# Kernel optimization log

Hardware: AMD Instinct MI355X
Metric: run time of the kernel (lower is better)

The kernel has to match this reference:

```python
import jax, jax.numpy as jnp
import numpy as np

B, T, D, K = 16, 4096, 512, 128
ALPHA_MIN = 1e-06
OMEGA_MAX = float(np.pi)
SN_EPS = 1e-06


def setup_inputs() -> dict:
    key = jax.random.key(0)
    ks = jax.random.split(key, 7)
    x = jax.random.normal(ks[0], (B, T, D), jnp.float32)
    # irregular positive step sizes, mean ~ 1/T like the uniform-grid default
    dt = jax.random.uniform(ks[1], (B, T), jnp.float32, minval=0.1, maxval=1.9) * (1.0 / T)
    # replicate reset_parameters: target_alpha ~ U(0.01, 0.2), raw = log(expm1(alpha - alpha_min))
    target_alpha = jax.random.uniform(ks[2], (K,), jnp.float32, minval=0.01, maxval=0.2)
    s_real_raw = jnp.log(jnp.expm1(jnp.maximum(target_alpha - ALPHA_MIN, 1e-08)))
    s_imag = jax.random.uniform(ks[3], (K,), jnp.float32, minval=-np.pi, maxval=np.pi)
    # kaiming-uniform-ish proj weight [K, D] and bias [K]
    W = jax.random.normal(ks[4], (K, D), jnp.float32) * (1.0 / np.sqrt(D))
    bound = 1.0 / np.sqrt(D)
    bias = jax.random.uniform(ks[5], (K,), jnp.float32, minval=-bound, maxval=bound)
    b_log = jnp.zeros((K,), jnp.float32)  # torch stores [1,1,K]; broadcasting is identical
    u_sn = jax.random.normal(ks[6], (K,), jnp.float32)  # spectral-norm power-iteration vector
    return {"x": x, "dt": dt, "s_real_raw": s_real_raw, "s_imag": s_imag,
            "W": W, "bias": bias, "b_log": b_log, "u_sn": u_sn}


def _spectral_normalize(W, u):
    # one power iteration, u/v detached (as torch.nn.utils.spectral_norm does)
    v = W.T @ u
    v = v / (jnp.linalg.norm(v) + SN_EPS)
    u2 = W @ v
    u2 = u2 / (jnp.linalg.norm(u2) + SN_EPS)
    u2 = jax.lax.stop_gradient(u2)
    v = jax.lax.stop_gradient(v)
    sigma = u2 @ (W @ v)
    return W / sigma


def reference(x, dt, s_real_raw, s_imag, W, bias, b_log, u_sn):
    # x: [B,T,D], dt: [B,T] -> lap_feats [B,T,2K]
    alpha = jax.nn.softplus(s_real_raw) + ALPHA_MIN          # [K] strictly positive decay
    omega = jnp.clip(s_imag, -OMEGA_MAX, OMEGA_MAX)          # [K]
    Wsn = _spectral_normalize(W, u_sn)
    u = jnp.einsum('btd,kd->btk', x, Wsn) + bias             # spectral-norm projection
    dt3 = dt[..., None]                                      # [B,T,1]
    rho = jnp.exp(-alpha * dt3)                              # [B,T,K]
    theta = omega * dt3
    cos_t, sin_t = jnp.cos(theta), jnp.sin(theta)
    b_gain = jnp.exp(b_log)                                  # [K]
    inj = (1.0 - rho) * (b_gain * u)                         # [B,T,K]

    def step(carry, inp):
        c, s = carry
        r, ct, st, it = inp
        c_new = r * (c * ct - s * st) + it
        s_new = r * (c * st + s * ct) + it
        return (c_new, s_new), (c_new, s_new)

    seq = (jnp.moveaxis(rho, 1, 0), jnp.moveaxis(cos_t, 1, 0),
           jnp.moveaxis(sin_t, 1, 0), jnp.moveaxis(inj, 1, 0))  # each [T,B,K]
    init = (jnp.zeros((x.shape[0], K), x.dtype), jnp.zeros((x.shape[0], K), x.dtype))
    _, (C, S) = jax.lax.scan(step, init, seq)
    C = jnp.moveaxis(C, 0, 1)  # [B,T,K]
    S = jnp.moveaxis(S, 0, 1)
    return jnp.concatenate([C, S], axis=-1)
```

## Files before the change

### kernel.cpp

```cpp
#include <hip/hip_runtime.h>
#include <stdint.h>

#define BB 16
#define TT 4096
#define DDIM 512
#define KK 128
#define TCB 128
#define NCB (TT / TCB)
#define PI_F 3.14159265358979323846f

typedef unsigned short u16;
typedef __attribute__((ext_vector_type(8))) short short8;
typedef __attribute__((ext_vector_type(4))) float f32x4;

__device__ __forceinline__ uint32_t cvt_bf16_rn(float f) {
  uint32_t u = __float_as_uint(f);
  return (u + 0x7FFFu + ((u >> 16) & 1u)) >> 16;
}
__device__ __forceinline__ uint32_t pack2(float a, float b) {
  return cvt_bf16_rn(a) | (cvt_bf16_rn(b) << 16);
}
__device__ __forceinline__ short8 pack8s(float4 f0, float4 f1) {
  uint4 u;
  u.x = pack2(f0.x, f0.y);
  u.y = pack2(f0.z, f0.w);
  u.z = pack2(f1.x, f1.y);
  u.w = pack2(f1.z, f1.w);
  return __builtin_bit_cast(short8, u);
}

__global__ __launch_bounds__(256) void k_prep(
    const float* __restrict__ W, const float* __restrict__ u_sn,
    const float* __restrict__ s_real_raw, const float* __restrict__ s_imag,
    const float* __restrict__ bias, const float* __restrict__ b_log,
    const float* __restrict__ dt,
    float* __restrict__ params, u16* __restrict__ Wp2, float* __restrict__ ct) {
  int gb = blockIdx.x;
  int tid = threadIdx.x;
  if (gb < 64) {
    int idx = gb * 256 + tid;
    int o = idx * 4;
    int lent = o >> 3;
    int half = (o >> 2) & 1;
    int ks = lent >> 9;
    int rem = lent & 511;
    int kg = rem >> 6;
    int l = rem & 63;
    int k = kg * 16 + (l & 15);
    int d = ks * 32 + (l >> 4) * 8 + half * 4;
    float4 v = *(const float4*)&W[(size_t)k * DDIM + d];
    uint2 p;
    p.x = pack2(v.x, v.y);
    p.y = pack2(v.z, v.w);
    *(uint2*)&Wp2[o] = p;
  } else if (gb < 80) {
    __shared__ float sc[256];
    int b = gb - 64;
    const float* row = dt + (size_t)b * TT;
    float* orow = ct + (size_t)b * TT;
    float loc[16];
    float s = 0.f;
    int base = tid * 16;
    for (int i = 0; i < 16; ++i) { s += row[base + i]; loc[i] = s; }
    sc[tid] = s;
    __syncthreads();
    for (int off = 1; off < 256; off <<= 1) {
      float v = (tid >= off) ? sc[tid - off] : 0.f;
      __syncthreads();
      sc[tid] += v;
      __syncthreads();
    }
    float excl = sc[tid] - s;
    for (int i = 0; i < 16; ++i) orow[base + i] = excl + loc[i];
  } else {
    __shared__ float su[KK];
    __shared__ float sv[DDIM];
    __shared__ float red[4];
    __shared__ float wred[256];
    __shared__ float s_sig;
    if (tid < KK) su[tid] = u_sn[tid];
    __syncthreads();
    for (int rep = 0; rep < 2; ++rep) {
      int d = tid + rep * 256;
      float acc = 0.f;
      for (int k = 0; k < KK; ++k) acc += W[k * DDIM + d] * su[k];
      sv[d] = acc;
    }
    __syncthreads();
    float nn = 0.f;
    for (int rep = 0; rep < 2; ++rep) { float v = sv[tid + rep * 256]; nn += v * v; }
    for (int off = 32; off > 0; off >>= 1) nn += __shfl_down(nn, off, 64);
    if ((tid & 63) == 0) red[tid >> 6] = nn;
    __syncthreads();
    float vn2 = red[0] + red[1] + red[2] + red[3];
    __syncthreads();
    float vinv = 1.f / (sqrtf(vn2) + 1e-6f);
    for (int rep = 0; rep < 2; ++rep) sv[tid + rep * 256] *= vinv;
    __syncthreads();
    {
      int k = tid & 127, q = tid >> 7;
      const float* wrow = W + (size_t)k * DDIM + q * 256;
      float p = 0.f;
      for (int d = 0; d < 256; ++d) p += wrow[d] * sv[q * 256 + d];
      wred[tid] = p;
    }
    __syncthreads();
    float wv = 0.f;
    if (tid < KK) wv = wred[tid] + wred[tid + 128];
    float q = wv * wv;
    for (int off = 32; off > 0; off >>= 1) q += __shfl_down(q, off, 64);
    if ((tid & 63) == 0) red[tid >> 6] = q;
    __syncthreads();
    if (tid == 0) {
      float wn2 = red[0] + red[1] + red[2] + red[3];
      s_sig = wn2 / (sqrtf(wn2) + 1e-6f);
    }
    __syncthreads();
    if (tid < KK) {
      float inv_sigma = 1.f / s_sig;
      float sr = s_real_raw[tid];
      float alpha = ((sr > 20.f) ? sr : log1pf(expf(sr))) + 1e-6f;
      float om = fminf(fmaxf(s_imag[tid], -PI_F), PI_F);
      float bg = expf(b_log[tid]);
      params[tid] = alpha;
      params[KK + tid] = om;
      params[2 * KK + tid] = bg * inv_sigma;
      params[3 * KK + tid] = bg * bias[tid];
    }
  }
}

__global__ __launch_bounds__(512, 4) void k_gemm(
    const float* __restrict__ x, const u16* __restrict__ Wp2,
    const float* __restrict__ dt, const float* __restrict__ ct,
    const float* __restrict__ params, u16* __restrict__ itvb,
    float* __restrict__ csum_re, float* __restrict__ csum_im) {
  __shared__ __align__(16) u16 smem[18432];

  const int chunk = blockIdx.x, b = blockIdx.y;
  const int tid = threadIdx.x;
  const int wv = tid >> 6, l = tid & 63;
  const int lm = l & 15, lg = l >> 4;
  const int kw = wv & 1, tw = wv >> 1;
  const int t0 = chunk * TCB;

  const float* xA0 = x + ((size_t)b * TT + t0 + tw * 32 + lm) * DDIM + lg * 8;
  const float* xA1 = xA0 + (size_t)16 * DDIM;
  const u16* wB = Wp2 + (size_t)(kw * 4) * 512 + l * 8;

  f32x4 acc[2][4];
#pragma unroll
  for (int m = 0; m < 2; ++m)
#pragma unroll
    for (int n = 0; n < 4; ++n) acc[m][n] = (f32x4)(0.0f);

#pragma unroll 4
  for (int ks = 0; ks < 16; ++ks) {
    float4 a00 = *(const float4*)(xA0 + ks * 32);
    float4 a01 = *(const float4*)(xA0 + ks * 32 + 4);
    float4 a10 = *(const float4*)(xA1 + ks * 32);
    float4 a11 = *(const float4*)(xA1 + ks * 32 + 4);
    short8 fb[4];
#pragma unroll
    for (int n = 0; n < 4; ++n)
      fb[n] = *(const short8*)(wB + (size_t)(ks * 8 + n) * 512);
    short8 fa[2];
    fa[0] = pack8s(a00, a01);
    fa[1] = pack8s(a10, a11);
#pragma unroll
    for (int m = 0; m < 2; ++m)
#pragma unroll
      for (int n = 0; n < 4; ++n)
        acc[m][n] = __builtin_amdgcn_mfma_f32_16x16x32_bf16(fa[m], fb[n], acc[m][n], 0, 0, 0);
  }

  u16* litv = smem;
  float* totr = (float*)(smem + 16384);
  float* toti = totr + 512;

  float dtv[2][4], ctv[2][4];
#pragma unroll
  for (int m = 0; m < 2; ++m)
#pragma unroll
    for (int r = 0; r < 4; ++r) {
      int t = t0 + tw * 32 + m * 16 + lg * 4 + r;
      dtv[m][r] = dt[(size_t)b * TT + t];
      ctv[m][r] = ct[(size_t)b * TT + t];
    }

#pragma unroll
  for (int n = 0; n < 4; ++n) {
    int k = kw * 64 + n * 16 + lm;
    float pal = params[k], pom = params[KK + k];
    float pc1 = params[2 * KK + k], pc2 = params[3 * KK + k];
    float sr = 0.f, si2 = 0.f;
#pragma unroll
    for (int m = 0; m < 2; ++m)
#pragma unroll
      for (int r = 0; r < 4; ++r) {
        float g = acc[m][n][r];
        float a = pal * dtv[m][r];
        float omr = a * (1.f - a * (0.5f - a * (1.f / 6.f)));
        float itv = omr * (pc1 * g + pc2);
        int tl = tw * 32 + m * 16 + lg * 4 + r;
        litv[tl * KK + k] = (u16)cvt_bf16_rn(itv);
        float e = __expf(pal * ctv[m][r]);
        float sn, cs;
        __sincosf(pom * ctv[m][r], &sn, &cs);
        sr += itv * e * cs;
        si2 -= itv * e * sn;
      }
    sr += __shfl_xor(sr, 16, 64);
    sr += __shfl_xor(sr, 32, 64);
    si2 += __shfl_xor(si2, 16, 64);
    si2 += __shfl_xor(si2, 32, 64);
    if (lg == 0) { totr[tw * KK + k] = sr; toti[tw * KK + k] = si2; }
  }
  __syncthreads();

  if (tid < 256) {
    int v = tid & 127;
    float* src = (tid < 128) ? totr : toti;
    float* dst = (tid < 128) ? csum_re : csum_im;
    dst[((size_t)b * NCB + chunk) * KK + v] =
        (src[v] + src[KK + v]) + (src[2 * KK + v] + src[3 * KK + v]);
  }
  {
    int row = tid >> 4;
    int c8 = (tid & 15) * 8;
#pragma unroll
    for (int rr = 0; rr < 4; ++rr) {
      int tr = rr * 32 + row;
      uint4 v = *(const uint4*)&litv[tr * KK + c8];
      *(uint4*)&itvb[((size_t)b * TT + t0 + tr) * KK + c8] = v;
    }
  }
}

__global__ __launch_bounds__(512) void k_final(
    const u16* __restrict__ itvb, const float* __restrict__ ct,
    const float* __restrict__ params,
    const float* __restrict__ csum_re, const float* __restrict__ csum_im,
    float* __restrict__ out) {
  __shared__ float prer[KK], prei[KK];
  __shared__ float segr[16][KK], segi[16][KK];
  const int chunk = blockIdx.x, b = blockIdx.y;
  const int tid = threadIdx.x;
  const int k4 = (tid & 31) * 4, tseg = tid >> 5;
  const int tbase = chunk * TCB + tseg * 8;

  if (tid < 256) {
    int v = tid & 127;
    const float* srcp = (tid < 128) ? csum_re : csum_im;
    float* dstp = (tid < 128) ? prer : prei;
    size_t base = (size_t)b * NCB * KK + v;
    float a0 = 0.f, a1 = 0.f, a2 = 0.f, a3 = 0.f;
    int c = 0;
    for (; c + 4 <= chunk; c += 4) {
      a0 += srcp[base + (size_t)(c + 0) * KK];
      a1 += srcp[base + (size_t)(c + 1) * KK];
      a2 += srcp[base + (size_t)(c + 2) * KK];
      a3 += srcp[base + (size_t)(c + 3) * KK];
    }
    for (; c < chunk; ++c) a0 += srcp[base + (size_t)c * KK];
    dstp[v] = (a0 + a1) + (a2 + a3);
  }

  float4 pal4 = *(const float4*)&params[k4];
  float4 pom4 = *(const float4*)&params[KK + k4];
  float pal[4] = {pal4.x, pal4.y, pal4.z, pal4.w};
  float pom[4] = {pom4.x, pom4.y, pom4.z, pom4.w};

  uint2 iv8[8];
  float fr[8][4], fi[8][4];
  float sr[4] = {0.f, 0.f, 0.f, 0.f}, si[4] = {0.f, 0.f, 0.f, 0.f};
#pragma unroll
  for (int i = 0; i < 8; ++i) {
    int t = tbase + i;
    float ctv = ct[(size_t)b * TT + t];
    iv8[i] = *(const uint2*)&itvb[((size_t)b * TT + t) * KK + k4];
    float it[4] = {__uint_as_float(iv8[i].x << 16), __uint_as_float(iv8[i].x & 0xFFFF0000u),
                   __uint_as_float(iv8[i].y << 16), __uint_as_float(iv8[i].y & 0xFFFF0000u)};
#pragma unroll
    for (int c = 0; c < 4; ++c) {
      float e = __expf(pal[c] * ctv);
      float sn, cs;
      __sincosf(pom[c] * ctv, &sn, &cs);
      fr[i][c] = e * cs;
      fi[i][c] = e * sn;
      sr[c] += it[c] * fr[i][c];
      si[c] -= it[c] * fi[i][c];
    }
  }
  *(float4*)&segr[tseg][k4] = make_float4(sr[0], sr[1], sr[2], sr[3]);
  *(float4*)&segi[tseg][k4] = make_float4(si[0], si[1], si[2], si[3]);
  __syncthreads();
  float cr[4], ci[4];
  {
    float4 p0 = *(const float4*)&prer[k4];
    float4 p1 = *(const float4*)&prei[k4];
    cr[0] = p0.x; cr[1] = p0.y; cr[2] = p0.z; cr[3] = p0.w;
    ci[0] = p1.x; ci[1] = p1.y; ci[2] = p1.z; ci[3] = p1.w;
  }
  for (int s = 0; s < tseg; ++s) {
    float4 a = *(const float4*)&segr[s][k4];
    float4 bb = *(const float4*)&segi[s][k4];
    cr[0] += a.x; cr[1] += a.y; cr[2] += a.z; cr[3] += a.w;
    ci[0] += bb.x; ci[1] += bb.y; ci[2] += bb.z; ci[3] += bb.w;
  }
#pragma unroll
  for (int i = 0; i < 8; ++i) {
    int t = tbase + i;
    float it[4] = {__uint_as_float(iv8[i].x << 16), __uint_as_float(iv8[i].x & 0xFFFF0000u),
                   __uint_as_float(iv8[i].y << 16), __uint_as_float(iv8[i].y & 0xFFFF0000u)};
    float C4[4], S4[4];
#pragma unroll
    for (int c = 0; c < 4; ++c) {
      float f_r = fr[i][c], f_i = fi[i][c];
      cr[c] += it[c] * f_r;
      ci[c] -= it[c] * f_i;
      float inv = __builtin_amdgcn_rcpf(f_r * f_r + f_i * f_i);
      float Rw = (cr[c] * f_r - ci[c] * f_i) * inv;
      float Iw = (cr[c] * f_i + ci[c] * f_r) * inv;
      C4[c] = Rw - Iw;
      S4[c] = Rw + Iw;
    }
    size_t rowb = ((size_t)b * TT + t) * (2 * KK);
    *(float4*)&out[rowb + k4] = make_float4(C4[0], C4[1], C4[2], C4[3]);
    *(float4*)&out[rowb + KK + k4] = make_float4(S4[0], S4[1], S4[2], S4[3]);
  }
}

extern "C" void kernel_launch(void* const* d_in, const int* in_sizes, int n_in,
                              void* d_out, int out_size, void* d_ws, size_t ws_size,
                              hipStream_t stream) {
  const float* x    = (const float*)d_in[0];
  const float* dt   = (const float*)d_in[1];
  const float* srr  = (const float*)d_in[2];
  const float* si   = (const float*)d_in[3];
  const float* W    = (const float*)d_in[4];
  const float* bias = (const float*)d_in[5];
  const float* blog = (const float*)d_in[6];
  const float* usn  = (const float*)d_in[7];
  float* out = (float*)d_out;
  float* ws = (float*)d_ws;

  float* params  = ws;
  float* ct      = ws + 4 * KK;
  float* csum_re = ct + (size_t)BB * TT;
  float* csum_im = csum_re + (size_t)BB * NCB * KK;
  u16*   Wp2     = (u16*)(csum_im + (size_t)BB * NCB * KK);
  u16*   itvb    = Wp2 + 65536;

  k_prep<<<81, 256, 0, stream>>>(W, usn, srr, si, bias, blog, dt, params, Wp2, ct);
  k_gemm<<<dim3(NCB, BB), 512, 0, stream>>>(x, Wp2, dt, ct, params, itvb,
                                            csum_re, csum_im);
  k_final<<<dim3(NCB, BB), 512, 0, stream>>>(itvb, ct, params,
                                             csum_re, csum_im, out);
}
```

Measured before the change: 82.67 us.

## Stage x tile in swizzled LDS and halve GEMM chunk size

The GEMM kernel now takes 64-timestep chunks instead of 128, which doubles its grid, and splits K across four waves instead of two. Each block first loads its x tile with coalesced reads, converts it to bf16 and writes it to LDS with an XOR swizzle. The MFMA loop then reads A fragments from LDS instead of doing strided global loads per lane. The final kernel keeps 128-step chunks and sums twice as many partial carry chunks. This costs more LDS per block (64KB) and two extra barriers, which may lower occupancy.

```diff
diff --git a/kernel.cpp b/kernel.cpp
--- a/kernel.cpp
+++ b/kernel.cpp
@@ -5,8 +5,10 @@
 #define TT 4096
 #define DDIM 512
 #define KK 128
-#define TCB 128
-#define NCB (TT / TCB)
+#define TCA 64
+#define NCA (TT / TCA)
+#define TCF 128
+#define NCF (TT / TCF)
 #define PI_F 3.14159265358979323846f
 
 typedef unsigned short u16;
@@ -20,13 +22,13 @@
 __device__ __forceinline__ uint32_t pack2(float a, float b) {
   return cvt_bf16_rn(a) | (cvt_bf16_rn(b) << 16);
 }
-__device__ __forceinline__ short8 pack8s(float4 f0, float4 f1) {
+__device__ __forceinline__ uint4 pack8u(float4 f0, float4 f1) {
   uint4 u;
   u.x = pack2(f0.x, f0.y);
   u.y = pack2(f0.z, f0.w);
   u.z = pack2(f1.x, f1.y);
   u.w = pack2(f1.z, f1.w);
-  return __builtin_bit_cast(short8, u);
+  return u;
 }
 
 __global__ __launch_bounds__(256) void k_prep(
@@ -135,48 +137,60 @@
     const float* __restrict__ dt, const float* __restrict__ ct,
     const float* __restrict__ params, u16* __restrict__ itvb,
     float* __restrict__ csum_re, float* __restrict__ csum_im) {
-  __shared__ __align__(16) u16 smem[18432];
-
-  const int chunk = blockIdx.x, b = blockIdx.y;
+  __shared__ __align__(16) u16 smem[32768];
+
+  const int ca = blockIdx.x, b = blockIdx.y;
   const int tid = threadIdx.x;
   const int wv = tid >> 6, l = tid & 63;
   const int lm = l & 15, lg = l >> 4;
-  const int kw = wv & 1, tw = wv >> 1;
-  const int t0 = chunk * TCB;
-
-  const float* xA0 = x + ((size_t)b * TT + t0 + tw * 32 + lm) * DDIM + lg * 8;
-  const float* xA1 = xA0 + (size_t)16 * DDIM;
-  const u16* wB = Wp2 + (size_t)(kw * 4) * 512 + l * 8;
-
-  f32x4 acc[2][4];
+  const int kw = wv & 3, tw = wv >> 2;
+  const int t0 = ca * TCA;
+
+  {
+    const float* xb0 = x + ((size_t)b * TT + t0) * DDIM;
+#pragma unroll
+    for (int i = 0; i < 8; ++i) {
+      int g = i * 512 + tid;
+      int t = g >> 6, c8 = g & 63;
+      int tile = c8 >> 3, dl8 = c8 & 7;
+      float4 v0 = *(const float4*)(xb0 + (size_t)t * DDIM + c8 * 8);
+      float4 v1 = *(const float4*)(xb0 + (size_t)t * DDIM + c8 * 8 + 4);
+      *(uint4*)&smem[tile * 4096 + t * 64 + ((dl8 ^ (t & 7)) << 3)] = pack8u(v0, v1);
+    }
+  }
+  __syncthreads();
+
+  f32x4 acc[2][2];
 #pragma unroll
   for (int m = 0; m < 2; ++m)
 #pragma unroll
-    for (int n = 0; n < 4; ++n) acc[m][n] = (f32x4)(0.0f);
-
+    for (int n = 0; n < 2; ++n) acc[m][n] = (f32x4)(0.0f);
+
+  const u16* wB = Wp2 + (size_t)(kw * 2) * 512 + l * 8;
 #pragma unroll 4
   for (int ks = 0; ks < 16; ++ks) {
-    float4 a00 = *(const float4*)(xA0 + ks * 32);
-    float4 a01 = *(const float4*)(xA0 + ks * 32 + 4);
-    float4 a10 = *(const float4*)(xA1 + ks * 32);
-    float4 a11 = *(const float4*)(xA1 + ks * 32 + 4);
-    short8 fb[4];
-#pragma unroll
-    for (int n = 0; n < 4; ++n)
+    short8 fb[2];
+#pragma unroll
+    for (int n = 0; n < 2; ++n)
       fb[n] = *(const short8*)(wB + (size_t)(ks * 8 + n) * 512);
     short8 fa[2];
-    fa[0] = pack8s(a00, a01);
-    fa[1] = pack8s(a10, a11);
+#pragma unroll
+    for (int m = 0; m < 2; ++m) {
+      int row = tw * 32 + m * 16 + lm;
+      int sw = (((ks & 1) * 4 + lg) ^ (row & 7)) * 8;
+      fa[m] = *(const short8*)&smem[(ks >> 1) * 4096 + row * 64 + sw];
+    }
 #pragma unroll
     for (int m = 0; m < 2; ++m)
 #pragma unroll
-      for (int n = 0; n < 4; ++n)
+      for (int n = 0; n < 2; ++n)
         acc[m][n] = __builtin_amdgcn_mfma_f32_16x16x32_bf16(fa[m], fb[n], acc[m][n], 0, 0, 0);
   }
+  __syncthreads();
 
   u16* litv = smem;
-  float* totr = (float*)(smem + 16384);
-  float* toti = totr + 512;
+  float* totr = (float*)(smem + 8192);
+  float* toti = totr + 256;
 
   float dtv[2][4], ctv[2][4];
 #pragma unroll
@@ -189,8 +203,8 @@
     }
 
 #pragma unroll
-  for (int n = 0; n < 4; ++n) {
-    int k = kw * 64 + n * 16 + lm;
+  for (int n = 0; n < 2; ++n) {
+    int k = kw * 32 + n * 16 + lm;
     float pal = params[k], pom = params[KK + k];
     float pc1 = params[2 * KK + k], pc2 = params[3 * KK + k];
     float sr = 0.f, si2 = 0.f;
@@ -222,14 +236,13 @@
     int v = tid & 127;
     float* src = (tid < 128) ? totr : toti;
     float* dst = (tid < 128) ? csum_re : csum_im;
-    dst[((size_t)b * NCB + chunk) * KK + v] =
-        (src[v] + src[KK + v]) + (src[2 * KK + v] + src[3 * KK + v]);
+    dst[((size_t)b * NCA + ca) * KK + v] = src[v] + src[KK + v];
   }
   {
     int row = tid >> 4;
     int c8 = (tid & 15) * 8;
 #pragma unroll
-    for (int rr = 0; rr < 4; ++rr) {
+    for (int rr = 0; rr < 2; ++rr) {
       int tr = rr * 32 + row;
       uint4 v = *(const uint4*)&litv[tr * KK + c8];
       *(uint4*)&itvb[((size_t)b * TT + t0 + tr) * KK + c8] = v;
@@ -247,22 +260,23 @@
   const int chunk = blockIdx.x, b = blockIdx.y;
   const int tid = threadIdx.x;
   const int k4 = (tid & 31) * 4, tseg = tid >> 5;
-  const int tbase = chunk * TCB + tseg * 8;
+  const int tbase = chunk * TCF + tseg * 8;
 
   if (tid < 256) {
     int v = tid & 127;
     const float* srcp = (tid < 128) ? csum_re : csum_im;
     float* dstp = (tid < 128) ? prer : prei;
-    size_t base = (size_t)b * NCB * KK + v;
+    size_t base = (size_t)b * NCA * KK + v;
+    int lim = 2 * chunk;
     float a0 = 0.f, a1 = 0.f, a2 = 0.f, a3 = 0.f;
     int c = 0;
-    for (; c + 4 <= chunk; c += 4) {
+    for (; c + 4 <= lim; c += 4) {
       a0 += srcp[base + (size_t)(c + 0) * KK];
       a1 += srcp[base + (size_t)(c + 1) * KK];
       a2 += srcp[base + (size_t)(c + 2) * KK];
       a3 += srcp[base + (size_t)(c + 3) * KK];
     }
-    for (; c < chunk; ++c) a0 += srcp[base + (size_t)c * KK];
+    for (; c < lim; ++c) a0 += srcp[base + (size_t)c * KK];
     dstp[v] = (a0 + a1) + (a2 + a3);
   }
 
@@ -348,13 +362,13 @@
   float* params  = ws;
   float* ct      = ws + 4 * KK;
   float* csum_re = ct + (size_t)BB * TT;
-  float* csum_im = csum_re + (size_t)BB * NCB * KK;
-  u16*   Wp2     = (u16*)(csum_im + (size_t)BB * NCB * KK);
+  float* csum_im = csum_re + (size_t)BB * NCA * KK;
+  u16*   Wp2     = (u16*)(csum_im + (size_t)BB * NCA * KK);
   u16*   itvb    = Wp2 + 65536;
 
   k_prep<<<81, 256, 0, stream>>>(W, usn, srr, si, bias, blog, dt, params, Wp2, ct);
-  k_gemm<<<dim3(NCB, BB), 512, 0, stream>>>(x, Wp2, dt, ct, params, itvb,
+  k_gemm<<<dim3(NCA, BB), 512, 0, stream>>>(x, Wp2, dt, ct, params, itvb,
                                             csum_re, csum_im);
-  k_final<<<dim3(NCB, BB), 512, 0, stream>>>(itvb, ct, params,
+  k_final<<<dim3(NCF, BB), 512, 0, stream>>>(itvb, ct, params,
                                              csum_re, csum_im, out);
 }
```

Result: faster. 77.64 us (-6.1%).
